# Optimization experiments

Hardware: AMD Instinct MI355X
Metric: run time of the kernel (lower is better)

Reference implementation:

```python
import jax, jax.numpy as jnp
import numpy as np

D = 256      # n_feature
LVL = 17     # tree depth (leaf levels)
MIX = 20     # M mixture components


def _lstm_cell(x, h, c, Wih, Whh, bih, bhh):
    # torch.nn.LSTMCell gate order: i, f, g, o
    g = x @ Wih.T + bih + h @ Whh.T + bhh
    i, f, gg, o = jnp.split(g, 4, axis=1)
    c2 = jax.nn.sigmoid(f) * c + jax.nn.sigmoid(i) * jnp.tanh(gg)
    return jax.nn.sigmoid(o) * jnp.tanh(c2), c2


def _get_parameter(y, M):
    parts = jnp.split(y[:, :13 * M], 13, axis=1)
    pi = jax.nn.softmax(parts[0], axis=1)
    mu_x, mu_y = parts[1], parts[2]
    sx, sy = jnp.exp(parts[3]), jnp.exp(parts[4])
    rho_xy = jnp.tanh(parts[5])
    mu_a, mu_b = parts[6], parts[7]
    sa, sb = jnp.exp(parts[8]), jnp.exp(parts[9])
    rho_ab = jnp.tanh(parts[10])
    mu_s, ss = parts[11], jnp.exp(parts[12])
    q = jax.nn.softmax(y[:, -3:], axis=1)
    return (pi, mu_x, mu_y, sx, sy, rho_xy, mu_a, mu_b, sa, sb, rho_ab, mu_s, ss, q)


def _bvn_logpdf(dx, dy, mx, my, sx, sy, rho):
    zx = (dx - mx) / sx
    zy = (dy - my) / sy
    Z = zx ** 2 + zy ** 2 - 2.0 * rho * zx * zy
    return -Z / (2.0 * (1.0 - rho ** 2)) - jnp.log(2.0 * jnp.pi * sx * sy * jnp.sqrt(1.0 - rho ** 2))


def _nll(pt, prm):
    # pt: [n, 8] = (x, y, a, b, slope, p1, p2, p3); prm: GMM parameters, each [n, M]
    pi, mx, my, sx, sy, rxy, ma, mb, sa, sb, rab, ms, ss, q = prm
    lpi = jnp.log(pi)
    dx, dy, da, db, ds = (pt[:, k:k + 1] for k in range(5))
    p = pt[:, 5:8]
    lse = jax.scipy.special.logsumexp
    lxy = lse(lpi + _bvn_logpdf(dx, dy, mx, my, sx, sy, rxy), axis=1)
    lab = lse(lpi + _bvn_logpdf(da, db, ma, mb, sa, sb, rab), axis=1)
    lsl = lse(lpi - (ds - ms) ** 2 / (2.0 * ss ** 2) - jnp.log(jnp.sqrt(2.0 * jnp.pi) * ss), axis=1)
    pen = -(p * jnp.log(q)).sum(axis=1)
    return -(lxy + lab + lsl) + pen


def _expected_pos(prm):
    pi, mx, my, sx, sy, rxy, ma, mb, sa, sb, rab, ms, ss, q = prm
    e = lambda m: (pi * m).sum(axis=1)
    return jnp.concatenate([jnp.stack([e(mx), e(my), e(ma), e(mb), e(ms)], axis=1), q], axis=1)


def _levels(I_flat):
    # I_flat is bottom-up concatenation of per-level [ni,3] blocks of a full binary tree
    n_int = I_flat.shape[0]
    L = int(np.log2(n_int + 1))
    sizes = [2 ** (L - 1 - i) for i in range(L)]
    offs = np.concatenate([[0], np.cumsum(sizes)])
    return [I_flat[offs[i]:offs[i + 1]] for i in range(L)]


def setup_inputs() -> dict:
    key = jax.random.key(0)
    ks = jax.random.split(key, 16)
    N = 2 ** (LVL + 1) - 1  # 262143 total nodes
    # heap-layout full binary tree: children of i are 2i+1, 2i+2; bottom-up levels
    blocks = []
    for l in range(LVL - 1, -1, -1):
        f = np.arange(2 ** l - 1, 2 ** (l + 1) - 1)
        blocks.append(np.stack([2 * f + 1, 2 * f + 2, f], axis=1))
    I_flat = jnp.asarray(np.concatenate(blocks, 0), dtype=jnp.int32)
    s = 0.05
    return {
        "X": jax.random.normal(ks[0], (N, 8), jnp.float32),
        "Feature": jax.random.normal(ks[1], (N, D), jnp.float32),
        "I_flat": I_flat,
        "W_ih_e": jax.random.normal(ks[2], (4 * (D // 2), 8), jnp.float32) * s,
        "W_hh_e": jax.random.normal(ks[3], (4 * (D // 2), D // 2), jnp.float32) * s,
        "b_ih_e": jax.random.normal(ks[4], (4 * (D // 2),), jnp.float32) * s,
        "b_hh_e": jax.random.normal(ks[5], (4 * (D // 2),), jnp.float32) * s,
        "fc_h_W": jax.random.normal(ks[6], (2 * D, D), jnp.float32) * s,
        "fc_h_b": jax.random.normal(ks[7], (2 * D,), jnp.float32) * s,
        "W_ih_d": jax.random.normal(ks[8], (4 * D, D + 8), jnp.float32) * s,
        "W_hh_d": jax.random.normal(ks[9], (4 * D, D), jnp.float32) * s,
        "b_ih_d": jax.random.normal(ks[10], (4 * D,), jnp.float32) * s,
        "b_hh_d": jax.random.normal(ks[11], (4 * D,), jnp.float32) * s,
        "fc_W": jax.random.normal(ks[12], (13 * MIX + 3, D // 2), jnp.float32) * s,
        "fc_b": jax.random.normal(ks[13], (13 * MIX + 3,), jnp.float32) * s,
    }


def reference(X, Feature, I_flat, W_ih_e, W_hh_e, b_ih_e, b_hh_e,
              fc_h_W, fc_h_b, W_ih_d, W_hh_d, b_ih_d, b_hh_d, fc_W, fc_b):
    levels = _levels(I_flat)
    num_I = len(levels)

    # ---- encode: bottom-up gather children -> LSTMCell -> scatter father ----
    Feature_New = Feature
    for I in levels:
        li, ri, fi = I[:, 0], I[:, 1], I[:, 2]
        hl, cl = jnp.split(Feature[li], 2, axis=1)
        hr, cr = jnp.split(Feature[ri], 2, axis=1)
        hlo, clo = _lstm_cell(X[li], hl, cl, W_ih_e, W_hh_e, b_ih_e, b_hh_e)
        hro, cro = _lstm_cell(X[ri], hr, cr, W_ih_e, W_hh_e, b_ih_e, b_hh_e)
        out = jnp.concatenate([hlo + hro, clo + cro], axis=1)
        Feature_New = Feature_New.at[fi].set(out)

    # ---- decode: top-down gather father -> LSTMCell+GMM head -> scatter children ----
    X_P = X
    Feat = Feature_New
    Loss = jnp.float32(0.0)
    for I in reversed(levels):
        li, ri, fi = I[:, 0], I[:, 1], I[:, 2]
        p_l, p_r, p_f = X[li], X[ri], X[fi]
        f_f = Feat[fi]
        z = jnp.tanh(f_f @ fc_h_W.T + fc_h_b)
        h_f, c_f = jnp.split(z, 2, axis=1)
        h_o, c_o = _lstm_cell(jnp.concatenate([p_f, f_f], axis=1), h_f, c_f,
                              W_ih_d, W_hh_d, b_ih_d, b_hh_d)
        h_left, h_right = jnp.split(h_o, 2, axis=1)
        c_left, c_right = jnp.split(c_o, 2, axis=1)
        prm_l = _get_parameter(h_left @ fc_W.T + fc_b, MIX)
        prm_r = _get_parameter(h_right @ fc_W.T + fc_b, MIX)
        direct = _nll(p_l, prm_l) + _nll(p_r, prm_r)
        swapped = _nll(p_l, prm_r) + _nll(p_r, prm_l)
        sw = swapped < direct  # l_r_index == 1 -> swap left/right outputs
        Loss = Loss + jnp.mean(jnp.where(sw, swapped, direct))
        pos_l, pos_r = _expected_pos(prm_l), _expected_pos(prm_r)
        feat_l = jnp.concatenate([h_left, c_left], axis=1)
        feat_r = jnp.concatenate([h_right, c_right], axis=1)
        swc = sw[:, None]
        Feat = Feat.at[li].set(jnp.where(swc, feat_r, feat_l))
        Feat = Feat.at[ri].set(jnp.where(swc, feat_l, feat_r))
        X_P = X_P.at[li].set(jnp.where(swc, pos_r, pos_l))
        X_P = X_P.at[ri].set(jnp.where(swc, pos_l, pos_r))
    return Loss / num_I
```

## Files before the change

kernel.cpp:

```cpp
#include <hip/hip_runtime.h>
#include <hip/hip_bf16.h>
#include <math.h>


#define LOG2PI 1.8378770664093453f

typedef __attribute__((ext_vector_type(8))) short short8;
typedef __attribute__((ext_vector_type(4))) float f32x4;

__device__ inline float sigm(float x) { return 1.0f / (1.0f + expf(-x)); }

__device__ inline ushort f2b(float v) {
    union { float f; unsigned u; } x; x.f = v;
    unsigned r = x.u + 0x7fffu + ((x.u >> 16) & 1u);
    return (ushort)(r >> 16);
}
__device__ inline float b2f(ushort h) {
    union { unsigned u; float f; } x; x.u = ((unsigned)h) << 16; return x.f;
}

__device__ inline void gload16(const void* g, void* l) {
    __builtin_amdgcn_global_load_lds(
        (const __attribute__((address_space(1))) unsigned*)g,
        (__attribute__((address_space(3))) unsigned*)l, 16, 0, 0);
}

template <int ACT, int OUT_MODE>
__global__ __launch_bounds__(256) void gemm_bf16(
    const ushort* __restrict__ A, int lda, int Mclamp,
    const ushort* __restrict__ B, int ldb, int Nclamp,
    const float* __restrict__ bias0, const float* __restrict__ bias1,
    float* __restrict__ Cf, ushort* __restrict__ Cb, int ldc,
    int M, int N, int K)
{
    __shared__ ushort As[128 * 64];
    __shared__ ushort Bs[128 * 64];
    const int tid = threadIdx.x;
    const int lane = tid & 63;
    const int w = tid >> 6;
    const int wr = w >> 1, wc = w & 1;
    const int fr = lane & 15, fq = lane >> 4;
    const int m0 = blockIdx.x * 128, n0 = blockIdx.y * 128;

    f32x4 acc[4][4] = {};

    for (int k0 = 0; k0 < K; k0 += 64) {
        __syncthreads();
        #pragma unroll
        for (int it = 0; it < 4; ++it) {
            const int i = it * 256 + tid;
            const int row = i >> 3, slot = i & 7;
            const int sl = slot ^ (row & 7);
            const int wbase = (i - lane) * 8;
            {
                int gm = m0 + row; gm = gm <= Mclamp ? gm : Mclamp;
                gload16(A + (size_t)gm * lda + k0 + sl * 8, &As[wbase]);
            }
            {
                int gn = n0 + row; gn = gn <= Nclamp ? gn : Nclamp;
                gload16(B + (size_t)gn * ldb + k0 + sl * 8, &Bs[wbase]);
            }
        }
        __syncthreads();
        #pragma unroll
        for (int ks = 0; ks < 2; ++ks) {
            short8 af[4], bfr[4];
            #pragma unroll
            for (int mr = 0; mr < 4; ++mr) {
                const int row = wr * 64 + mr * 16 + fr;
                const int sl = (ks * 4 + fq) ^ (row & 7);
                af[mr] = *(const short8*)&As[row * 64 + sl * 8];
            }
            #pragma unroll
            for (int nc = 0; nc < 4; ++nc) {
                const int row = wc * 64 + nc * 16 + fr;
                const int sl = (ks * 4 + fq) ^ (row & 7);
                bfr[nc] = *(const short8*)&Bs[row * 64 + sl * 8];
            }
            #pragma unroll
            for (int mr = 0; mr < 4; ++mr)
                #pragma unroll
                for (int nc = 0; nc < 4; ++nc)
                    acc[mr][nc] = __builtin_amdgcn_mfma_f32_16x16x32_bf16(
                        af[mr], bfr[nc], acc[mr][nc], 0, 0, 0);
        }
    }

    #pragma unroll
    for (int mr = 0; mr < 4; ++mr) {
        #pragma unroll
        for (int j = 0; j < 4; ++j) {
            const int row = m0 + wr * 64 + mr * 16 + fq * 4 + j;
            if (row >= M) continue;
            #pragma unroll
            for (int nc = 0; nc < 4; ++nc) {
                const int col = n0 + wc * 64 + nc * 16 + fr;
                if (col >= N) continue;
                float v = acc[mr][nc][j] + bias0[col] + (bias1 ? bias1[col] : 0.f);
                if (ACT == 1) v = tanhf(v);
                if (OUT_MODE == 0) Cf[(size_t)row * ldc + col] = v;
                else               Cb[(size_t)row * ldc + col] = f2b(v);
            }
        }
    }
}

__global__ __launch_bounds__(256) void gates_lstm(
    const ushort* __restrict__ Xb,
    const ushort* __restrict__ Fcur,
    const ushort* __restrict__ Zb,
    const ushort* __restrict__ Wg,
    const float*  __restrict__ bg,
    ushort* __restrict__ H, ushort* __restrict__ C, int M)
{
    __shared__ ushort As[128 * 64];
    __shared__ ushort Bs[128 * 64];
    const int tid = threadIdx.x;
    const int lane = tid & 63;
    const int w = tid >> 6;
    const int wr = w >> 1, wc = w & 1;
    const int fr = lane & 15, fq = lane >> 4;
    const int m0 = blockIdx.x * 128, n0 = blockIdx.y * 128;

    f32x4 acc[4][4] = {};

    for (int k0 = 0; k0 < 576; k0 += 64) {
        __syncthreads();
        const int sbase = k0 >> 3;
        #pragma unroll
        for (int it = 0; it < 4; ++it) {
            const int i = it * 256 + tid;
            const int row = i >> 3, slot = i & 7;
            const int sl = slot ^ (row & 7);
            const int wbase = (i - lane) * 8;
            {
                int gm = m0 + row; gm = gm < M ? gm : M - 1;
                const int a = sbase + sl;
                const ushort* src;
                if (a == 0)      src = Xb   + (size_t)gm * 8;
                else if (a < 33) src = Fcur + (size_t)gm * 256 + (size_t)(a - 1) * 8;
                else if (a < 65) src = Zb   + (size_t)gm * 512 + (size_t)(a - 33) * 8;
                else             src = Zb   + (size_t)gm * 512;
                gload16(src, &As[wbase]);
            }
            gload16(Wg + (size_t)(n0 + row) * 576 + k0 + sl * 8, &Bs[wbase]);
        }
        __syncthreads();
        #pragma unroll
        for (int ks = 0; ks < 2; ++ks) {
            short8 af[4], bfr[4];
            #pragma unroll
            for (int mr = 0; mr < 4; ++mr) {
                const int row = wr * 64 + mr * 16 + fr;
                const int sl = (ks * 4 + fq) ^ (row & 7);
                af[mr] = *(const short8*)&As[row * 64 + sl * 8];
            }
            #pragma unroll
            for (int nc = 0; nc < 4; ++nc) {
                const int row = wc * 64 + nc * 16 + fr;
                const int sl = (ks * 4 + fq) ^ (row & 7);
                bfr[nc] = *(const short8*)&Bs[row * 64 + sl * 8];
            }
            #pragma unroll
            for (int mr = 0; mr < 4; ++mr)
                #pragma unroll
                for (int nc = 0; nc < 4; ++nc)
                    acc[mr][nc] = __builtin_amdgcn_mfma_f32_16x16x32_bf16(
                        af[mr], bfr[nc], acc[mr][nc], 0, 0, 0);
        }
    }

    const int q = fr & 3;
    #pragma unroll
    for (int mr = 0; mr < 4; ++mr) {
        const int node = m0 + wr * 64 + mr * 16 + fq * 4 + q;
        #pragma unroll
        for (int nc = 0; nc < 4; ++nc) {
            const int col = n0 + wc * 64 + nc * 16 + fr;
            f32x4 v = acc[mr][nc];
            const float b = bg[col];
            v[0] += b; v[1] += b; v[2] += b; v[3] += b;
            float gv[4];
            gv[q] = v[q];
            #pragma unroll
            for (int m = 1; m < 4; ++m)
                gv[q ^ m] = __shfl_xor(v[q ^ m], m);
            if (node < M) {
                const int t = (col >> 2) & 255;
                const float cf = b2f(Zb[(size_t)node * 512 + 256 + t]);
                const float c2 = sigm(gv[1]) * cf + sigm(gv[0]) * tanhf(gv[2]);
                const float hv = sigm(gv[3]) * tanhf(c2);
                H[(size_t)node * 256 + t] = f2b(hv);
                C[(size_t)node * 256 + t] = f2b(c2);
            }
        }
    }
}

__global__ __launch_bounds__(256) void conv_f2b(const float* __restrict__ s,
                                                ushort* __restrict__ d, int n)
{
    int i = blockIdx.x * 256 + threadIdx.x;
    if (i < n) d[i] = f2b(s[i]);
}
__global__ __launch_bounds__(256) void pack_wg(const float* __restrict__ Wih,
                                               const float* __restrict__ Whh,
                                               ushort* __restrict__ d)
{
    int i = blockIdx.x * 256 + threadIdx.x;
    if (i >= 1024 * 576) return;
    int np = i / 576, c = i % 576;
    int n = (np & 3) * 256 + (np >> 2);
    float v = 0.f;
    if (c < 264) v = Wih[n * 264 + c];
    else if (c < 520) v = Whh[n * 256 + (c - 264)];
    d[i] = f2b(v);
}
__global__ __launch_bounds__(256) void pack_bg(const float* __restrict__ bih,
                                               const float* __restrict__ bhh,
                                               float* __restrict__ d)
{
    int np = blockIdx.x * 256 + threadIdx.x;
    if (np >= 1024) return;
    int n = (np & 3) * 256 + (np >> 2);
    d[np] = bih[n] + bhh[n];
}
__global__ __launch_bounds__(256) void pack_wy(const float* __restrict__ W,
                                               ushort* __restrict__ d)
{
    int i = blockIdx.x * 256 + threadIdx.x;
    if (i >= 320 * 128) return;
    int r = i / 128;
    d[i] = f2b(r < 263 ? W[i] : 0.f);
}

__global__ __launch_bounds__(256) void encoder_root(
    const float* __restrict__ X, const float* __restrict__ Feature,
    const float* __restrict__ Wih, const float* __restrict__ Whh,
    const float* __restrict__ bih, const float* __restrict__ bhh,
    ushort* __restrict__ Fcur0)
{
    __shared__ float gsh[2][512];
    __shared__ float hc[2][256];
    const int t = threadIdx.x;
    for (int ch = 0; ch < 2; ++ch) {
        const int node = 1 + ch;
        const float* x = X + node * 8;
        const float* h = Feature + (size_t)node * 256;
        #pragma unroll
        for (int gi = 0; gi < 2; ++gi) {
            int g = t + gi * 256;
            float s = bih[g] + bhh[g];
            const float* wi = Wih + (size_t)g * 8;
            #pragma unroll
            for (int k = 0; k < 8; ++k) s += wi[k] * x[k];
            const float* wh = Whh + (size_t)g * 128;
            for (int k = 0; k < 128; ++k) s += wh[k] * h[k];
            gsh[ch][g] = s;
        }
    }
    __syncthreads();
    {
        int ch = t >> 7, u = t & 127;
        float i_ = gsh[ch][u], f_ = gsh[ch][128 + u];
        float gg = gsh[ch][256 + u], o_ = gsh[ch][384 + u];
        float c = Feature[(size_t)(1 + ch) * 256 + 128 + u];
        float c2 = sigm(f_) * c + sigm(i_) * tanhf(gg);
        hc[ch][u] = sigm(o_) * tanhf(c2);
        hc[ch][128 + u] = c2;
    }
    __syncthreads();
    Fcur0[t] = f2b(hc[0][t] + hc[1][t]);
}

__device__ inline float halfmax(float v) {
    #pragma unroll
    for (int o = 16; o >= 1; o >>= 1) v = fmaxf(v, __shfl_xor(v, o));
    return v;
}
__device__ inline float halfsum(float v) {
    #pragma unroll
    for (int o = 16; o >= 1; o >>= 1) v += __shfl_xor(v, o);
    return v;
}
__device__ inline float lse20(float t) {
    float m = halfmax(t);
    float s = halfsum(expf(t - m));
    return m + logf(s);
}

__global__ __launch_bounds__(256) void ynll(
    const ushort* __restrict__ Hb, const ushort* __restrict__ Cc,
    const ushort* __restrict__ Wyp,
    const float* __restrict__ fc_b, const float* __restrict__ X,
    ushort* __restrict__ FeatNext, float* __restrict__ loss,
    int Bc, long long nb, int j0, float scale, int writeFeat)
{
    __shared__ ushort Hs[32 * 128];
    __shared__ float Ys[32][324];
    __shared__ float lsum[4];
    const int tid = threadIdx.x;
    const int lane = tid & 63;
    const int wv = tid >> 6;
    const int fr = lane & 15, fq = lane >> 4;
    const int n16 = blockIdx.x * 16;

    #pragma unroll
    for (int it = 0; it < 2; ++it) {
        const int i = it * 256 + tid;
        const int row = i >> 4, slot = i & 15;
        const int sl = slot ^ (row & 7);
        int gr = n16 * 2 + row;
        const int grmax = 2 * Bc - 1;
        gr = gr <= grmax ? gr : grmax;
        gload16(Hb + (size_t)gr * 128 + sl * 8, &Hs[(i - lane) * 8]);
    }
    __syncthreads();

    f32x4 acc[2][5] = {};
    #pragma unroll
    for (int ks = 0; ks < 4; ++ks) {
        short8 a[2];
        #pragma unroll
        for (int rf = 0; rf < 2; ++rf) {
            const int row = rf * 16 + fr;
            const int sl = (ks * 4 + fq) ^ (row & 7);
            a[rf] = *(const short8*)&Hs[row * 128 + sl * 8];
        }
        #pragma unroll
        for (int n = 0; n < 5; ++n) {
            const short8 b = *(const short8*)(
                Wyp + (size_t)(wv * 80 + n * 16 + fr) * 128 + ks * 32 + fq * 8);
            acc[0][n] = __builtin_amdgcn_mfma_f32_16x16x32_bf16(a[0], b, acc[0][n], 0, 0, 0);
            acc[1][n] = __builtin_amdgcn_mfma_f32_16x16x32_bf16(a[1], b, acc[1][n], 0, 0, 0);
        }
    }
    #pragma unroll
    for (int rf = 0; rf < 2; ++rf)
        #pragma unroll
        for (int n = 0; n < 5; ++n)
            #pragma unroll
            for (int j = 0; j < 4; ++j) {
                const int row = rf * 16 + fq * 4 + j;
                const int col = wv * 80 + n * 16 + fr;
                Ys[row][col] = acc[rf][n][j] + (col < 263 ? fc_b[col] : 0.f);
            }
    __syncthreads();

    float wsum = 0.f;
    const int half = lane >> 5, k = lane & 31;
    #pragma unroll
    for (int s4 = 0; s4 < 4; ++s4) {
        const int jj = wv * 4 + s4;
        const int j = n16 + jj;
        if (j >= Bc) break;
        const float* yb = Ys[2 * jj + half];
        float v = (k < 20) ? yb[k] : -INFINITY;
        float mm = halfmax(v);
        float se = halfsum((k < 20) ? expf(v - mm) : 0.f);
        float lpi = v - mm - logf(se);
        float mx = 0, my = 0, sx = 1, sy = 1, rho = 0, omr = 1, cxy = 0;
        float ma = 0, mb2 = 0, sa = 1, sb = 1, rab = 0, omr2 = 1, cab = 0;
        float ms = 0, ss2 = 1, csl = 0;
        if (k < 20) {
            mx = yb[20 + k]; my = yb[40 + k];
            float lsx = yb[60 + k], lsy = yb[80 + k];
            sx = expf(lsx); sy = expf(lsy);
            rho = tanhf(yb[100 + k]); omr = 1.f - rho * rho;
            cxy = LOG2PI + lsx + lsy + 0.5f * logf(omr);
            ma = yb[120 + k]; mb2 = yb[140 + k];
            float lsa = yb[160 + k], lsb = yb[180 + k];
            sa = expf(lsa); sb = expf(lsb);
            rab = tanhf(yb[200 + k]); omr2 = 1.f - rab * rab;
            cab = LOG2PI + lsa + lsb + 0.5f * logf(omr2);
            ms = yb[220 + k]; float lss = yb[240 + k];
            ss2 = expf(lss);
            csl = 0.5f * LOG2PI + lss;
        }
        float lq0, lq1, lq2;
        {
            float q0 = yb[260], q1 = yb[261], q2 = yb[262];
            float qm = fmaxf(q0, fmaxf(q1, q2));
            float l = logf(expf(q0 - qm) + expf(q1 - qm) + expf(q2 - qm)) + qm;
            lq0 = q0 - l; lq1 = q1 - l; lq2 = q2 - l;
        }
        const long long fi = nb + j0 + j;
        const float* pl = X + (size_t)(2 * fi + 1) * 8;
        const float* pr = X + (size_t)(2 * fi + 2) * 8;
        float res[2];
        #pragma unroll
        for (int s = 0; s < 2; ++s) {
            const float* pt = s ? pr : pl;
            float dx = pt[0], dy = pt[1], da = pt[2], db = pt[3], ds = pt[4];
            float t1 = -INFINITY, t2 = -INFINITY, t3 = -INFINITY;
            if (k < 20) {
                float zx = (dx - mx) / sx, zy = (dy - my) / sy;
                float Zz = zx * zx + zy * zy - 2.f * rho * zx * zy;
                t1 = lpi - Zz / (2.f * omr) - cxy;
                float za = (da - ma) / sa, zb = (db - mb2) / sb;
                float Z2 = za * za + zb * zb - 2.f * rab * za * zb;
                t2 = lpi - Z2 / (2.f * omr2) - cab;
                float zs = ds - ms;
                t3 = lpi - (zs * zs) / (2.f * ss2 * ss2) - csl;
            }
            float l1 = lse20(t1), l2 = lse20(t2), l3 = lse20(t3);
            float pen = -(pt[5] * lq0 + pt[6] * lq1 + pt[7] * lq2);
            res[s] = -(l1 + l2 + l3) + pen;
        }
        float Aval = half ? res[1] : res[0];
        float Bval = half ? res[0] : res[1];
        float direct = Aval + __shfl_xor(Aval, 32);
        float swapped = Bval + __shfl_xor(Bval, 32);
        bool sw = swapped < direct;
        wsum += sw ? swapped : direct;
        if (writeFeat) {
            const size_t Jg = 2 * (size_t)(j0 + j);
            const ushort* Hj = Hb + (size_t)j * 256;
            const ushort* Cj = Cc + (size_t)j * 256;
            const int offL = sw ? 128 : 0;
            const int offR = 128 - offL;
            const int part = lane >> 5;
            const int c = (lane & 31) * 4;
            ushort4 vL = *(const ushort4*)((part ? Cj : Hj) + offL + c);
            ushort4 vR = *(const ushort4*)((part ? Cj : Hj) + offR + c);
            *(ushort4*)(FeatNext + Jg * 256 + part * 128 + c) = vL;
            *(ushort4*)(FeatNext + (Jg + 1) * 256 + part * 128 + c) = vR;
        }
    }
    if (lane == 0) lsum[wv] = wsum;
    __syncthreads();
    if (tid == 0)
        atomicAdd(loss, (lsum[0] + lsum[1] + lsum[2] + lsum[3]) * scale);
}

extern "C" void kernel_launch(void* const* d_in, const int* in_sizes, int n_in,
                              void* d_out, int out_size, void* d_ws, size_t ws_size,
                              hipStream_t stream)
{
    const float* X       = (const float*)d_in[0];
    const float* Feature = (const float*)d_in[1];
    const float* W_ih_e  = (const float*)d_in[3];
    const float* W_hh_e  = (const float*)d_in[4];
    const float* b_ih_e  = (const float*)d_in[5];
    const float* b_hh_e  = (const float*)d_in[6];
    const float* fc_h_W  = (const float*)d_in[7];
    const float* fc_h_b  = (const float*)d_in[8];
    const float* W_ih_d  = (const float*)d_in[9];
    const float* W_hh_d  = (const float*)d_in[10];
    const float* b_ih_d  = (const float*)d_in[11];
    const float* b_hh_d  = (const float*)d_in[12];
    const float* fc_W    = (const float*)d_in[13];
    const float* fc_b    = (const float*)d_in[14];
    const int Nnodes = in_sizes[0] / 8;

    float* out = (float*)d_out;
    hipMemsetAsync(d_out, 0, sizeof(float), stream);

    char* cur = (char*)d_ws;
    auto take = [&](size_t bytes) {
        char* p = cur;
        cur += (bytes + 255) & ~(size_t)255;
        return p;
    };
    ushort* featA = (ushort*)take((size_t)65536 * 256 * 2);
    ushort* featB = (ushort*)take((size_t)32768 * 256 * 2);
    ushort* Wz    = (ushort*)take((size_t)512 * 256 * 2);
    ushort* Wg    = (ushort*)take((size_t)1024 * 576 * 2);
    ushort* Wy    = (ushort*)take((size_t)320 * 128 * 2);
    float*  bg    = (float*) take((size_t)1024 * 4);
    ushort* Xb    = (ushort*)take((size_t)Nnodes * 8 * 2);
    const size_t fixed_used = (size_t)(cur - (char*)d_ws);
    int CB = 65536;
    while (CB > 2048 && fixed_used + (size_t)CB * 2048 + 4096 > ws_size) CB >>= 1;
    ushort* Zb = (ushort*)take((size_t)CB * 512 * 2);
    ushort* Hb = (ushort*)take((size_t)CB * 256 * 2);
    ushort* Cc = (ushort*)take((size_t)CB * 256 * 2);

    conv_f2b<<<(512 * 256 + 255) / 256, 256, 0, stream>>>(fc_h_W, Wz, 512 * 256);
    pack_wg<<<(1024 * 576 + 255) / 256, 256, 0, stream>>>(W_ih_d, W_hh_d, Wg);
    pack_bg<<<4, 256, 0, stream>>>(b_ih_d, b_hh_d, bg);
    pack_wy<<<(320 * 128 + 255) / 256, 256, 0, stream>>>(fc_W, Wy);
    conv_f2b<<<(Nnodes * 8 + 255) / 256, 256, 0, stream>>>(X, Xb, Nnodes * 8);

    encoder_root<<<1, 256, 0, stream>>>(X, Feature, W_ih_e, W_hh_e, b_ih_e, b_hh_e, featA);

    for (int l = 0; l < 17; ++l) {
        const int B = 1 << l;
        const long long nb = B - 1;
        ushort* Fcur  = (l & 1) ? featB : featA;
        ushort* Fnext = (l & 1) ? featA : featB;
        const int writeFeat = (l < 16) ? 1 : 0;
        const float scale = 1.f / ((float)B * 17.f);
        for (int j0 = 0; j0 < B; j0 += CB) {
            const int Bc = (B - j0 < CB) ? (B - j0) : CB;
            const int mg = (Bc + 127) / 128;
            gemm_bf16<1, 1><<<dim3(mg, 4), 256, 0, stream>>>(
                Fcur + (size_t)j0 * 256, 256, Bc - 1,
                Wz, 256, 511,
                fc_h_b, nullptr, nullptr, Zb, 512, Bc, 512, 256);
            gates_lstm<<<dim3(mg, 8), 256, 0, stream>>>(
                Xb + (size_t)(nb + j0) * 8,
                Fcur + (size_t)j0 * 256,
                Zb, Wg, bg, Hb, Cc, Bc);
            ynll<<<(Bc + 15) / 16, 256, 0, stream>>>(
                Hb, Cc, Wy, fc_b, X,
                writeFeat ? Fnext : nullptr, out,
                Bc, nb, j0, scale, writeFeat);
        }
    }
}
```

Measured before the change: 1.463 ms.

## Stage gate-GEMM inputs in a persistent packed per-node A matrix

Adds one persistent packed bf16 operand buffer with 576 columns per internal node, holding X, the parent feature, z_h and zero padding. The z GEMM and the ynll kernel now write straight into this buffer, so the gates GEMM does one contiguous load per K slice instead of branching across three source pointers. The weight and X packing kernels are merged into one launch. The cost is a larger workspace sized to all internal nodes, extra scattered stores into 576-wide rows, and a larger minimum chunk size.

```diff
diff --git a/kernel.cpp b/kernel.cpp
--- a/kernel.cpp
+++ b/kernel.cpp
@@ -25,13 +25,110 @@
         (__attribute__((address_space(3))) unsigned*)l, 16, 0, 0);
 }
 
-template <int ACT, int OUT_MODE>
-__global__ __launch_bounds__(256) void gemm_bf16(
-    const ushort* __restrict__ A, int lda, int Mclamp,
-    const ushort* __restrict__ B, int ldb, int Nclamp,
-    const float* __restrict__ bias0, const float* __restrict__ bias1,
-    float* __restrict__ Cf, ushort* __restrict__ Cb, int ldc,
-    int M, int N, int K)
+__device__ inline f32x4 mfma16(short8 a, short8 b, f32x4 c) {
+    return __builtin_amdgcn_mfma_f32_16x16x32_bf16(a, b, c, 0, 0, 0);
+}
+
+__device__ inline float halfmax(float v) {
+    #pragma unroll
+    for (int o = 16; o >= 1; o >>= 1) v = fmaxf(v, __shfl_xor(v, o));
+    return v;
+}
+__device__ inline float halfsum(float v) {
+    #pragma unroll
+    for (int o = 16; o >= 1; o >>= 1) v += __shfl_xor(v, o);
+    return v;
+}
+__device__ inline float lse20(float t) {
+    float m = halfmax(t);
+    float s = halfsum(expf(t - m));
+    return m + logf(s);
+}
+
+__device__ inline float nll_node(const float* yb, const float* X,
+                                 long long fi, int lane, bool& sw_out)
+{
+    const int half = lane >> 5, k = lane & 31;
+    float v = (k < 20) ? yb[k] : -INFINITY;
+    float mm = halfmax(v);
+    float se = halfsum((k < 20) ? expf(v - mm) : 0.f);
+    float lpi = v - mm - logf(se);
+    float mx = 0, my = 0, sx = 1, sy = 1, rho = 0, omr = 1, cxy = 0;
+    float ma = 0, mb2 = 0, sa = 1, sb = 1, rab = 0, omr2 = 1, cab = 0;
+    float ms = 0, ss2 = 1, csl = 0;
+    if (k < 20) {
+        mx = yb[20 + k]; my = yb[40 + k];
+        float lsx = yb[60 + k], lsy = yb[80 + k];
+        sx = expf(lsx); sy = expf(lsy);
+        rho = tanhf(yb[100 + k]); omr = 1.f - rho * rho;
+        cxy = LOG2PI + lsx + lsy + 0.5f * logf(omr);
+        ma = yb[120 + k]; mb2 = yb[140 + k];
+        float lsa = yb[160 + k], lsb = yb[180 + k];
+        sa = expf(lsa); sb = expf(lsb);
+        rab = tanhf(yb[200 + k]); omr2 = 1.f - rab * rab;
+        cab = LOG2PI + lsa + lsb + 0.5f * logf(omr2);
+        ms = yb[220 + k]; float lss = yb[240 + k];
+        ss2 = expf(lss);
+        csl = 0.5f * LOG2PI + lss;
+    }
+    float lq0, lq1, lq2;
+    {
+        float q0 = yb[260], q1 = yb[261], q2 = yb[262];
+        float qm = fmaxf(q0, fmaxf(q1, q2));
+        float l = logf(expf(q0 - qm) + expf(q1 - qm) + expf(q2 - qm)) + qm;
+        lq0 = q0 - l; lq1 = q1 - l; lq2 = q2 - l;
+    }
+    const float* pl = X + (size_t)(2 * fi + 1) * 8;
+    const float* pr = X + (size_t)(2 * fi + 2) * 8;
+    float res[2];
+    #pragma unroll
+    for (int s = 0; s < 2; ++s) {
+        const float* pt = s ? pr : pl;
+        float dx = pt[0], dy = pt[1], da = pt[2], db = pt[3], ds = pt[4];
+        float t1 = -INFINITY, t2 = -INFINITY, t3 = -INFINITY;
+        if (k < 20) {
+            float zx = (dx - mx) / sx, zy = (dy - my) / sy;
+            float Zz = zx * zx + zy * zy - 2.f * rho * zx * zy;
+            t1 = lpi - Zz / (2.f * omr) - cxy;
+            float za = (da - ma) / sa, zb = (db - mb2) / sb;
+            float Z2 = za * za + zb * zb - 2.f * rab * za * zb;
+            t2 = lpi - Z2 / (2.f * omr2) - cab;
+            float zs = ds - ms;
+            t3 = lpi - (zs * zs) / (2.f * ss2 * ss2) - csl;
+        }
+        float l1 = lse20(t1), l2 = lse20(t2), l3 = lse20(t3);
+        float pen = -(pt[5] * lq0 + pt[6] * lq1 + pt[7] * lq2);
+        res[s] = -(l1 + l2 + l3) + pen;
+    }
+    float Aval = half ? res[1] : res[0];
+    float Bval = half ? res[0] : res[1];
+    float direct = Aval + __shfl_xor(Aval, 32);
+    float swapped = Bval + __shfl_xor(Bval, 32);
+    sw_out = swapped < direct;
+    return sw_out ? swapped : direct;
+}
+
+__device__ inline void feat_write_ap(ushort* Ap, const ushort* Hj,
+                                     const ushort* Cj, long long fi, bool sw,
+                                     int lane)
+{
+    const size_t rowL = 2 * (size_t)fi + 1;
+    const int offL = sw ? 128 : 0;
+    const int offR = 128 - offL;
+    const int part = lane >> 5;
+    const int c = (lane & 31) * 4;
+    ushort4 vL = *(const ushort4*)((part ? Cj : Hj) + offL + c);
+    ushort4 vR = *(const ushort4*)((part ? Cj : Hj) + offR + c);
+    *(ushort4*)(Ap + rowL * 576 + 8 + part * 128 + c) = vL;
+    *(ushort4*)(Ap + (rowL + 1) * 576 + 8 + part * 128 + c) = vR;
+}
+
+__global__ __launch_bounds__(256) void z_gemm(
+    ushort* __restrict__ Apc,
+    const ushort* __restrict__ Wz,
+    const float* __restrict__ fc_h_b,
+    ushort* __restrict__ Zcc,
+    int M)
 {
     __shared__ ushort As[128 * 64];
     __shared__ ushort Bs[128 * 64];
@@ -44,7 +141,8 @@
 
     f32x4 acc[4][4] = {};
 
-    for (int k0 = 0; k0 < K; k0 += 64) {
+    #pragma unroll
+    for (int k0 = 0; k0 < 256; k0 += 64) {
         __syncthreads();
         #pragma unroll
         for (int it = 0; it < 4; ++it) {
@@ -53,12 +151,12 @@
             const int sl = slot ^ (row & 7);
             const int wbase = (i - lane) * 8;
             {
-                int gm = m0 + row; gm = gm <= Mclamp ? gm : Mclamp;
-                gload16(A + (size_t)gm * lda + k0 + sl * 8, &As[wbase]);
+                int gm = m0 + row; gm = gm < M ? gm : M - 1;
+                gload16(Apc + (size_t)gm * 576 + 8 + k0 + sl * 8, &As[wbase]);
             }
             {
-                int gn = n0 + row; gn = gn <= Nclamp ? gn : Nclamp;
-                gload16(B + (size_t)gn * ldb + k0 + sl * 8, &Bs[wbase]);
+                int gn = n0 + row; gn = gn < 512 ? gn : 511;
+                gload16(Wz + (size_t)gn * 256 + k0 + sl * 8, &Bs[wbase]);
             }
         }
         __syncthreads();
@@ -81,8 +179,7 @@
             for (int mr = 0; mr < 4; ++mr)
                 #pragma unroll
                 for (int nc = 0; nc < 4; ++nc)
-                    acc[mr][nc] = __builtin_amdgcn_mfma_f32_16x16x32_bf16(
-                        af[mr], bfr[nc], acc[mr][nc], 0, 0, 0);
+                    acc[mr][nc] = mfma16(af[mr], bfr[nc], acc[mr][nc]);
         }
     }
 
@@ -95,22 +192,21 @@
             #pragma unroll
             for (int nc = 0; nc < 4; ++nc) {
                 const int col = n0 + wc * 64 + nc * 16 + fr;
-                if (col >= N) continue;
-                float v = acc[mr][nc][j] + bias0[col] + (bias1 ? bias1[col] : 0.f);
-                if (ACT == 1) v = tanhf(v);
-                if (OUT_MODE == 0) Cf[(size_t)row * ldc + col] = v;
-                else               Cb[(size_t)row * ldc + col] = f2b(v);
+                const float z = tanhf(acc[mr][nc][j] + fc_h_b[col]);
+                if (col < 256)
+                    Apc[(size_t)row * 576 + 264 + col] = f2b(z);
+                else
+                    Zcc[(size_t)row * 256 + (col - 256)] = f2b(z);
             }
         }
     }
 }
 
 __global__ __launch_bounds__(256) void gates_lstm(
-    const ushort* __restrict__ Xb,
-    const ushort* __restrict__ Fcur,
-    const ushort* __restrict__ Zb,
+    const ushort* __restrict__ Apc,
     const ushort* __restrict__ Wg,
     const float*  __restrict__ bg,
+    const ushort* __restrict__ Zcc,
     ushort* __restrict__ H, ushort* __restrict__ C, int M)
 {
     __shared__ ushort As[128 * 64];
@@ -124,9 +220,9 @@
 
     f32x4 acc[4][4] = {};
 
+    #pragma unroll
     for (int k0 = 0; k0 < 576; k0 += 64) {
         __syncthreads();
-        const int sbase = k0 >> 3;
         #pragma unroll
         for (int it = 0; it < 4; ++it) {
             const int i = it * 256 + tid;
@@ -135,13 +231,7 @@
             const int wbase = (i - lane) * 8;
             {
                 int gm = m0 + row; gm = gm < M ? gm : M - 1;
-                const int a = sbase + sl;
-                const ushort* src;
-                if (a == 0)      src = Xb   + (size_t)gm * 8;
-                else if (a < 33) src = Fcur + (size_t)gm * 256 + (size_t)(a - 1) * 8;
-                else if (a < 65) src = Zb   + (size_t)gm * 512 + (size_t)(a - 33) * 8;
-                else             src = Zb   + (size_t)gm * 512;
-                gload16(src, &As[wbase]);
+                gload16(Apc + (size_t)gm * 576 + k0 + sl * 8, &As[wbase]);
             }
             gload16(Wg + (size_t)(n0 + row) * 576 + k0 + sl * 8, &Bs[wbase]);
         }
@@ -165,8 +255,7 @@
             for (int mr = 0; mr < 4; ++mr)
                 #pragma unroll
                 for (int nc = 0; nc < 4; ++nc)
-                    acc[mr][nc] = __builtin_amdgcn_mfma_f32_16x16x32_bf16(
-                        af[mr], bfr[nc], acc[mr][nc], 0, 0, 0);
+                    acc[mr][nc] = mfma16(af[mr], bfr[nc], acc[mr][nc]);
         }
     }
 
@@ -187,7 +276,7 @@
                 gv[q ^ m] = __shfl_xor(v[q ^ m], m);
             if (node < M) {
                 const int t = (col >> 2) & 255;
-                const float cf = b2f(Zb[(size_t)node * 512 + 256 + t]);
+                const float cf = b2f(Zcc[(size_t)node * 256 + t]);
                 const float c2 = sigm(gv[1]) * cf + sigm(gv[0]) * tanhf(gv[2]);
                 const float hv = sigm(gv[3]) * tanhf(c2);
                 H[(size_t)node * 256 + t] = f2b(hv);
@@ -197,48 +286,129 @@
     }
 }
 
-__global__ __launch_bounds__(256) void conv_f2b(const float* __restrict__ s,
-                                                ushort* __restrict__ d, int n)
+__global__ __launch_bounds__(256) void ynll(
+    const ushort* __restrict__ Hb, const ushort* __restrict__ Cc,
+    const ushort* __restrict__ Wyp,
+    const float* __restrict__ fc_b, const float* __restrict__ X,
+    ushort* __restrict__ Ap, float* __restrict__ loss,
+    int Bc, long long nb_fi, float scale, int writeFeat)
+{
+    __shared__ ushort Hs[32 * 128];
+    __shared__ float Ys[32][324];
+    __shared__ float lsum[4];
+    const int tid = threadIdx.x;
+    const int lane = tid & 63;
+    const int wv = tid >> 6;
+    const int fr = lane & 15, fq = lane >> 4;
+    const int n16 = blockIdx.x * 16;
+
+    #pragma unroll
+    for (int it = 0; it < 2; ++it) {
+        const int i = it * 256 + tid;
+        const int row = i >> 4, slot = i & 15;
+        const int sl = slot ^ (row & 7);
+        int gr = n16 * 2 + row;
+        const int grmax = 2 * Bc - 1;
+        gr = gr <= grmax ? gr : grmax;
+        gload16(Hb + (size_t)gr * 128 + sl * 8, &Hs[(i - lane) * 8]);
+    }
+    __syncthreads();
+
+    f32x4 acc[2][5] = {};
+    #pragma unroll
+    for (int ks = 0; ks < 4; ++ks) {
+        short8 a[2];
+        #pragma unroll
+        for (int rf = 0; rf < 2; ++rf) {
+            const int row = rf * 16 + fr;
+            const int sl = (ks * 4 + fq) ^ (row & 7);
+            a[rf] = *(const short8*)&Hs[row * 128 + sl * 8];
+        }
+        #pragma unroll
+        for (int n = 0; n < 5; ++n) {
+            const short8 b = *(const short8*)(
+                Wyp + (size_t)(wv * 80 + n * 16 + fr) * 128 + ks * 32 + fq * 8);
+            acc[0][n] = mfma16(a[0], b, acc[0][n]);
+            acc[1][n] = mfma16(a[1], b, acc[1][n]);
+        }
+    }
+    #pragma unroll
+    for (int rf = 0; rf < 2; ++rf)
+        #pragma unroll
+        for (int n = 0; n < 5; ++n)
+            #pragma unroll
+            for (int j = 0; j < 4; ++j) {
+                const int row = rf * 16 + fq * 4 + j;
+                const int col = wv * 80 + n * 16 + fr;
+                Ys[row][col] = acc[rf][n][j] + (col < 263 ? fc_b[col] : 0.f);
+            }
+    __syncthreads();
+
+    float wsum = 0.f;
+    #pragma unroll
+    for (int s4 = 0; s4 < 4; ++s4) {
+        const int jj = wv * 4 + s4;
+        const int j = n16 + jj;
+        if (j >= Bc) break;
+        bool sw;
+        const long long fi = nb_fi + j;
+        wsum += nll_node(Ys[2 * jj + (lane >> 5)], X, fi, lane, sw);
+        if (writeFeat)
+            feat_write_ap(Ap, Hb + (size_t)j * 256, Cc + (size_t)j * 256,
+                          fi, sw, lane);
+    }
+    if (lane == 0) lsum[wv] = wsum;
+    __syncthreads();
+    if (tid == 0)
+        atomicAdd(loss, (lsum[0] + lsum[1] + lsum[2] + lsum[3]) * scale);
+}
+
+__global__ __launch_bounds__(256) void pack_all(
+    const float* __restrict__ fc_h_W, ushort* __restrict__ Wz,
+    const float* __restrict__ Wih, const float* __restrict__ Whh,
+    ushort* __restrict__ Wg,
+    const float* __restrict__ bih, const float* __restrict__ bhh,
+    float* __restrict__ bg,
+    const float* __restrict__ fcW, ushort* __restrict__ Wy,
+    const float* __restrict__ X, ushort* __restrict__ Ap, int nInt)
 {
     int i = blockIdx.x * 256 + threadIdx.x;
-    if (i < n) d[i] = f2b(s[i]);
-}
-__global__ __launch_bounds__(256) void pack_wg(const float* __restrict__ Wih,
-                                               const float* __restrict__ Whh,
-                                               ushort* __restrict__ d)
-{
-    int i = blockIdx.x * 256 + threadIdx.x;
-    if (i >= 1024 * 576) return;
-    int np = i / 576, c = i % 576;
-    int n = (np & 3) * 256 + (np >> 2);
-    float v = 0.f;
-    if (c < 264) v = Wih[n * 264 + c];
-    else if (c < 520) v = Whh[n * 256 + (c - 264)];
-    d[i] = f2b(v);
-}
-__global__ __launch_bounds__(256) void pack_bg(const float* __restrict__ bih,
-                                               const float* __restrict__ bhh,
-                                               float* __restrict__ d)
-{
-    int np = blockIdx.x * 256 + threadIdx.x;
-    if (np >= 1024) return;
-    int n = (np & 3) * 256 + (np >> 2);
-    d[np] = bih[n] + bhh[n];
-}
-__global__ __launch_bounds__(256) void pack_wy(const float* __restrict__ W,
-                                               ushort* __restrict__ d)
-{
-    int i = blockIdx.x * 256 + threadIdx.x;
-    if (i >= 320 * 128) return;
-    int r = i / 128;
-    d[i] = f2b(r < 263 ? W[i] : 0.f);
+    if (i < 131072) { Wz[i] = f2b(fc_h_W[i]); return; }
+    i -= 131072;
+    if (i < 589824) {
+        int np = i / 576, c = i - np * 576;
+        int n = (np & 3) * 256 + (np >> 2);
+        float v = 0.f;
+        if (c < 264) v = Wih[n * 264 + c];
+        else if (c < 520) v = Whh[n * 256 + (c - 264)];
+        Wg[i] = f2b(v);
+        return;
+    }
+    i -= 589824;
+    if (i < 1024) {
+        int n = (i & 3) * 256 + (i >> 2);
+        bg[i] = bih[n] + bhh[n];
+        return;
+    }
+    i -= 1024;
+    if (i < 40960) {
+        int r = i / 128;
+        Wy[i] = f2b(r < 263 ? fcW[i] : 0.f);
+        return;
+    }
+    i -= 40960;
+    if (i < nInt * 64) {
+        int row = i >> 6, c = i & 63;
+        if (c < 8) Ap[(size_t)row * 576 + c] = f2b(X[row * 8 + c]);
+        else       Ap[(size_t)row * 576 + 512 + c] = 0;
+    }
 }
 
 __global__ __launch_bounds__(256) void encoder_root(
     const float* __restrict__ X, const float* __restrict__ Feature,
     const float* __restrict__ Wih, const float* __restrict__ Whh,
     const float* __restrict__ bih, const float* __restrict__ bhh,
-    ushort* __restrict__ Fcur0)
+    ushort* __restrict__ Ap)
 {
     __shared__ float gsh[2][512];
     __shared__ float hc[2][256];
@@ -270,167 +440,7 @@
         hc[ch][128 + u] = c2;
     }
     __syncthreads();
-    Fcur0[t] = f2b(hc[0][t] + hc[1][t]);
-}
-
-__device__ inline float halfmax(float v) {
-    #pragma unroll
-    for (int o = 16; o >= 1; o >>= 1) v = fmaxf(v, __shfl_xor(v, o));
-    return v;
-}
-__device__ inline float halfsum(float v) {
-    #pragma unroll
-    for (int o = 16; o >= 1; o >>= 1) v += __shfl_xor(v, o);
-    return v;
-}
-__device__ inline float lse20(float t) {
-    float m = halfmax(t);
-    float s = halfsum(expf(t - m));
-    return m + logf(s);
-}
-
-__global__ __launch_bounds__(256) void ynll(
-    const ushort* __restrict__ Hb, const ushort* __restrict__ Cc,
-    const ushort* __restrict__ Wyp,
-    const float* __restrict__ fc_b, const float* __restrict__ X,
-    ushort* __restrict__ FeatNext, float* __restrict__ loss,
-    int Bc, long long nb, int j0, float scale, int writeFeat)
-{
-    __shared__ ushort Hs[32 * 128];
-    __shared__ float Ys[32][324];
-    __shared__ float lsum[4];
-    const int tid = threadIdx.x;
-    const int lane = tid & 63;
-    const int wv = tid >> 6;
-    const int fr = lane & 15, fq = lane >> 4;
-    const int n16 = blockIdx.x * 16;
-
-    #pragma unroll
-    for (int it = 0; it < 2; ++it) {
-        const int i = it * 256 + tid;
-        const int row = i >> 4, slot = i & 15;
-        const int sl = slot ^ (row & 7);
-        int gr = n16 * 2 + row;
-        const int grmax = 2 * Bc - 1;
-        gr = gr <= grmax ? gr : grmax;
-        gload16(Hb + (size_t)gr * 128 + sl * 8, &Hs[(i - lane) * 8]);
-    }
-    __syncthreads();
-
-    f32x4 acc[2][5] = {};
-    #pragma unroll
-    for (int ks = 0; ks < 4; ++ks) {
-        short8 a[2];
-        #pragma unroll
-        for (int rf = 0; rf < 2; ++rf) {
-            const int row = rf * 16 + fr;
-            const int sl = (ks * 4 + fq) ^ (row & 7);
-            a[rf] = *(const short8*)&Hs[row * 128 + sl * 8];
-        }
-        #pragma unroll
-        for (int n = 0; n < 5; ++n) {
-            const short8 b = *(const short8*)(
-                Wyp + (size_t)(wv * 80 + n * 16 + fr) * 128 + ks * 32 + fq * 8);
-            acc[0][n] = __builtin_amdgcn_mfma_f32_16x16x32_bf16(a[0], b, acc[0][n], 0, 0, 0);
-            acc[1][n] = __builtin_amdgcn_mfma_f32_16x16x32_bf16(a[1], b, acc[1][n], 0, 0, 0);
-        }
-    }
-    #pragma unroll
-    for (int rf = 0; rf < 2; ++rf)
-        #pragma unroll
-        for (int n = 0; n < 5; ++n)
-            #pragma unroll
-            for (int j = 0; j < 4; ++j) {
-                const int row = rf * 16 + fq * 4 + j;
-                const int col = wv * 80 + n * 16 + fr;
-                Ys[row][col] = acc[rf][n][j] + (col < 263 ? fc_b[col] : 0.f);
-            }
-    __syncthreads();
-
-    float wsum = 0.f;
-    const int half = lane >> 5, k = lane & 31;
-    #pragma unroll
-    for (int s4 = 0; s4 < 4; ++s4) {
-        const int jj = wv * 4 + s4;
-        const int j = n16 + jj;
-        if (j >= Bc) break;
-        const float* yb = Ys[2 * jj + half];
-        float v = (k < 20) ? yb[k] : -INFINITY;
-        float mm = halfmax(v);
-        float se = halfsum((k < 20) ? expf(v - mm) : 0.f);
-        float lpi = v - mm - logf(se);
-        float mx = 0, my = 0, sx = 1, sy = 1, rho = 0, omr = 1, cxy = 0;
-        float ma = 0, mb2 = 0, sa = 1, sb = 1, rab = 0, omr2 = 1, cab = 0;
-        float ms = 0, ss2 = 1, csl = 0;
-        if (k < 20) {
-            mx = yb[20 + k]; my = yb[40 + k];
-            float lsx = yb[60 + k], lsy = yb[80 + k];
-            sx = expf(lsx); sy = expf(lsy);
-            rho = tanhf(yb[100 + k]); omr = 1.f - rho * rho;
-            cxy = LOG2PI + lsx + lsy + 0.5f * logf(omr);
-            ma = yb[120 + k]; mb2 = yb[140 + k];
-            float lsa = yb[160 + k], lsb = yb[180 + k];
-            sa = expf(lsa); sb = expf(lsb);
-            rab = tanhf(yb[200 + k]); omr2 = 1.f - rab * rab;
-            cab = LOG2PI + lsa + lsb + 0.5f * logf(omr2);
-            ms = yb[220 + k]; float lss = yb[240 + k];
-            ss2 = expf(lss);
-            csl = 0.5f * LOG2PI + lss;
-        }
-        float lq0, lq1, lq2;
-        {
-            float q0 = yb[260], q1 = yb[261], q2 = yb[262];
-            float qm = fmaxf(q0, fmaxf(q1, q2));
-            float l = logf(expf(q0 - qm) + expf(q1 - qm) + expf(q2 - qm)) + qm;
-            lq0 = q0 - l; lq1 = q1 - l; lq2 = q2 - l;
-        }
-        const long long fi = nb + j0 + j;
-        const float* pl = X + (size_t)(2 * fi + 1) * 8;
-        const float* pr = X + (size_t)(2 * fi + 2) * 8;
-        float res[2];
-        #pragma unroll
-        for (int s = 0; s < 2; ++s) {
-            const float* pt = s ? pr : pl;
-            float dx = pt[0], dy = pt[1], da = pt[2], db = pt[3], ds = pt[4];
-            float t1 = -INFINITY, t2 = -INFINITY, t3 = -INFINITY;
-            if (k < 20) {
-                float zx = (dx - mx) / sx, zy = (dy - my) / sy;
-                float Zz = zx * zx + zy * zy - 2.f * rho * zx * zy;
-                t1 = lpi - Zz / (2.f * omr) - cxy;
-                float za = (da - ma) / sa, zb = (db - mb2) / sb;
-                float Z2 = za * za + zb * zb - 2.f * rab * za * zb;
-                t2 = lpi - Z2 / (2.f * omr2) - cab;
-                float zs = ds - ms;
-                t3 = lpi - (zs * zs) / (2.f * ss2 * ss2) - csl;
-            }
-            float l1 = lse20(t1), l2 = lse20(t2), l3 = lse20(t3);
-            float pen = -(pt[5] * lq0 + pt[6] * lq1 + pt[7] * lq2);
-            res[s] = -(l1 + l2 + l3) + pen;
-        }
-        float Aval = half ? res[1] : res[0];
-        float Bval = half ? res[0] : res[1];
-        float direct = Aval + __shfl_xor(Aval, 32);
-        float swapped = Bval + __shfl_xor(Bval, 32);
-        bool sw = swapped < direct;
-        wsum += sw ? swapped : direct;
-        if (writeFeat) {
-            const size_t Jg = 2 * (size_t)(j0 + j);
-            const ushort* Hj = Hb + (size_t)j * 256;
-            const ushort* Cj = Cc + (size_t)j * 256;
-            const int offL = sw ? 128 : 0;
-            const int offR = 128 - offL;
-            const int part = lane >> 5;
-            const int c = (lane & 31) * 4;
-            ushort4 vL = *(const ushort4*)((part ? Cj : Hj) + offL + c);
-            ushort4 vR = *(const ushort4*)((part ? Cj : Hj) + offR + c);
-            *(ushort4*)(FeatNext + Jg * 256 + part * 128 + c) = vL;
-            *(ushort4*)(FeatNext + (Jg + 1) * 256 + part * 128 + c) = vR;
-        }
-    }
-    if (lane == 0) lsum[wv] = wsum;
-    __syncthreads();
-    if (tid == 0)
-        atomicAdd(loss, (lsum[0] + lsum[1] + lsum[2] + lsum[3]) * scale);
+    Ap[8 + t] = f2b(hc[0][t] + hc[1][t]);
 }
 
 extern "C" void kernel_launch(void* const* d_in, const int* in_sizes, int n_in,
@@ -452,6 +462,7 @@
     const float* fc_W    = (const float*)d_in[13];
     const float* fc_b    = (const float*)d_in[14];
     const int Nnodes = in_sizes[0] / 8;
+    const int nInt = (Nnodes - 1) / 2;
 
     float* out = (float*)d_out;
     hipMemsetAsync(d_out, 0, sizeof(float), stream);
@@ -462,50 +473,41 @@
         cur += (bytes + 255) & ~(size_t)255;
         return p;
     };
-    ushort* featA = (ushort*)take((size_t)65536 * 256 * 2);
-    ushort* featB = (ushort*)take((size_t)32768 * 256 * 2);
-    ushort* Wz    = (ushort*)take((size_t)512 * 256 * 2);
-    ushort* Wg    = (ushort*)take((size_t)1024 * 576 * 2);
-    ushort* Wy    = (ushort*)take((size_t)320 * 128 * 2);
-    float*  bg    = (float*) take((size_t)1024 * 4);
-    ushort* Xb    = (ushort*)take((size_t)Nnodes * 8 * 2);
+    ushort* Ap = (ushort*)take((size_t)(nInt + 1) * 576 * 2);
+    ushort* Wz = (ushort*)take((size_t)512 * 256 * 2);
+    ushort* Wg = (ushort*)take((size_t)1024 * 576 * 2);
+    ushort* Wy = (ushort*)take((size_t)320 * 128 * 2);
+    float*  bg = (float*) take((size_t)1024 * 4);
     const size_t fixed_used = (size_t)(cur - (char*)d_ws);
     int CB = 65536;
-    while (CB > 2048 && fixed_used + (size_t)CB * 2048 + 4096 > ws_size) CB >>= 1;
-    ushort* Zb = (ushort*)take((size_t)CB * 512 * 2);
-    ushort* Hb = (ushort*)take((size_t)CB * 256 * 2);
-    ushort* Cc = (ushort*)take((size_t)CB * 256 * 2);
-
-    conv_f2b<<<(512 * 256 + 255) / 256, 256, 0, stream>>>(fc_h_W, Wz, 512 * 256);
-    pack_wg<<<(1024 * 576 + 255) / 256, 256, 0, stream>>>(W_ih_d, W_hh_d, Wg);
-    pack_bg<<<4, 256, 0, stream>>>(b_ih_d, b_hh_d, bg);
-    pack_wy<<<(320 * 128 + 255) / 256, 256, 0, stream>>>(fc_W, Wy);
-    conv_f2b<<<(Nnodes * 8 + 255) / 256, 256, 0, stream>>>(X, Xb, Nnodes * 8);
-
-    encoder_root<<<1, 256, 0, stream>>>(X, Feature, W_ih_e, W_hh_e, b_ih_e, b_hh_e, featA);
+    while (CB > 8192 && fixed_used + (size_t)CB * 1536 + 4096 > ws_size) CB >>= 1;
+    ushort* Zcc = (ushort*)take((size_t)CB * 256 * 2);
+    ushort* Hb  = (ushort*)take((size_t)CB * 256 * 2);
+    ushort* Cc  = (ushort*)take((size_t)CB * 256 * 2);
+
+    const int packTotal = 131072 + 589824 + 1024 + 40960 + nInt * 64;
+    pack_all<<<(packTotal + 255) / 256, 256, 0, stream>>>(
+        fc_h_W, Wz, W_ih_d, W_hh_d, Wg, b_ih_d, b_hh_d, bg, fc_W, Wy,
+        X, Ap, nInt);
+
+    encoder_root<<<1, 256, 0, stream>>>(X, Feature, W_ih_e, W_hh_e,
+                                        b_ih_e, b_hh_e, Ap);
 
     for (int l = 0; l < 17; ++l) {
         const int B = 1 << l;
         const long long nb = B - 1;
-        ushort* Fcur  = (l & 1) ? featB : featA;
-        ushort* Fnext = (l & 1) ? featA : featB;
         const int writeFeat = (l < 16) ? 1 : 0;
         const float scale = 1.f / ((float)B * 17.f);
         for (int j0 = 0; j0 < B; j0 += CB) {
             const int Bc = (B - j0 < CB) ? (B - j0) : CB;
             const int mg = (Bc + 127) / 128;
-            gemm_bf16<1, 1><<<dim3(mg, 4), 256, 0, stream>>>(
-                Fcur + (size_t)j0 * 256, 256, Bc - 1,
-                Wz, 256, 511,
-                fc_h_b, nullptr, nullptr, Zb, 512, Bc, 512, 256);
+            ushort* Apc = Ap + (size_t)(nb + j0) * 576;
+            z_gemm<<<dim3(mg, 4), 256, 0, stream>>>(Apc, Wz, fc_h_b, Zcc, Bc);
             gates_lstm<<<dim3(mg, 8), 256, 0, stream>>>(
-                Xb + (size_t)(nb + j0) * 8,
-                Fcur + (size_t)j0 * 256,
-                Zb, Wg, bg, Hb, Cc, Bc);
+                Apc, Wg, bg, Zcc, Hb, Cc, Bc);
             ynll<<<(Bc + 15) / 16, 256, 0, stream>>>(
-                Hb, Cc, Wy, fc_b, X,
-                writeFeat ? Fnext : nullptr, out,
-                Bc, nb, j0, scale, writeFeat);
-        }
-    }
-}
+                Hb, Cc, Wy, fc_b, X, Ap, out,
+                Bc, nb + j0, scale, writeFeat);
+        }
+    }
+}
```

New measurement: 1.459 ms. No clear change (-0.3%).
